# Optimization experiments

Hardware: AMD Instinct MI355X
Metric: run time of the kernel (lower is better)

Reference implementation:

```python
import jax, jax.numpy as jnp
import numpy as np
import math

B, L, NV, PRED = 8, 512, 32, 96
D, PL, STRIDE = 128, 16, 8
E, TOPN, H = 8, 2, 512
P = (L - PL) // STRIDE + 2  # 64 patches (includes replication pad of STRIDE)
BAL_COEF, Z_COEF = 0.01, 0.001


def sinusoid_pe(n, d):
    pos = np.arange(n, dtype=np.float32)[:, None]
    div = np.exp(np.arange(0, d, 2, dtype=np.float32) * -(math.log(10000.0) / d))
    pe = np.zeros((n, d), dtype=np.float32)
    pe[:, 0::2] = np.sin(pos * div)
    pe[:, 1::2] = np.cos(pos * div)
    return jnp.asarray(pe)


def setup_inputs() -> dict:
    key = jax.random.key(0)
    ks = jax.random.split(key, 10)
    return {
        "x_enc": jax.random.normal(ks[0], (B, L, NV), jnp.float32),
        "x_mark_enc": jax.random.normal(ks[1], (B, L, 4), jnp.float32),
        "x_dec": jnp.zeros((B, 144, NV), jnp.float32),
        "x_mark_dec": jnp.zeros((B, 144, 4), jnp.float32),
        "W_patch": jax.random.normal(ks[2], (PL, D), jnp.float32) * 0.05,
        "Wg": jax.random.normal(ks[3], (D, E), jnp.float32) * 0.05,
        "W1": jax.random.normal(ks[4], (E, D, H), jnp.float32) * 0.05,
        "b1": jnp.zeros((E, H), jnp.float32),
        "W2": jax.random.normal(ks[5], (E, H, D), jnp.float32) * 0.05,
        "b2": jnp.zeros((E, D), jnp.float32),
        "W_head": jax.random.normal(ks[6], (D * P, PRED), jnp.float32) * 0.02,
        "b_head": jnp.zeros((PRED,), jnp.float32),
    }


def _forward(x_enc, W_patch, Wg, W1, b1, W2, b2, W_head, b_head):
    # instance norm over time (detached stats, like the torch code)
    means = jax.lax.stop_gradient(jnp.mean(x_enc, axis=1, keepdims=True))
    xc = x_enc - means
    stdev = jax.lax.stop_gradient(
        jnp.sqrt(jnp.mean((x_enc - means) ** 2, axis=1, keepdims=True) + 1e-5))
    xc = xc / stdev
    # [B, NV, L] -> replication pad right by STRIDE -> unfold into patches
    x = jnp.transpose(xc, (0, 2, 1))
    xp = jnp.pad(x, ((0, 0), (0, 0), (0, STRIDE)), mode="edge")
    idx = jnp.arange(P)[:, None] * STRIDE + jnp.arange(PL)[None, :]  # [P, PL]
    patches = xp[:, :, idx]  # [B, NV, P, PL]
    tok = patches.reshape(B * NV, P, PL)
    h = jnp.einsum("tpl,ld->tpd", tok, W_patch) + sinusoid_pe(P, D)[None]
    # ---- MoE over flattened tokens ----
    N = B * NV * P
    xf = h.reshape(N, D)
    logits = xf @ Wg                              # [N, E]
    probs = jax.nn.softmax(logits, axis=-1)
    gates, tops = jax.lax.top_k(probs, TOPN)      # [N, TOPN]
    # dense per-expert FFN (exact GELU, as nn.GELU default)
    eh = jax.nn.gelu(jnp.einsum("nd,edh->neh", xf, W1) + b1, approximate=False)
    eo = jnp.einsum("neh,ehd->ned", eh, W2) + b2  # [N, E, D]
    onehot = jax.nn.one_hot(tops, E, dtype=xf.dtype)          # [N, TOPN, E]
    cw = jnp.einsum("nk,nke->ne", gates, onehot)              # combine weights
    y = jnp.einsum("ne,ned->nd", cw, eo)
    # aux losses: load-balance + router z-loss
    mask = onehot.sum(axis=1)                                  # [N, E]
    balance = E * jnp.sum(jnp.mean(probs, axis=0) * jnp.mean(mask, axis=0)) / TOPN
    zloss = jnp.mean(jax.nn.logsumexp(logits, axis=-1) ** 2)
    aux = BAL_COEF * balance + Z_COEF * zloss
    # ---- head ----
    enc = y.reshape(B, NV, P, D).transpose(0, 1, 3, 2)         # [B, NV, D, P]
    flat = enc.reshape(B, NV, D * P)
    dec = flat @ W_head + b_head                               # [B, NV, PRED]
    dec = jnp.transpose(dec, (0, 2, 1))                        # [B, PRED, NV]
    dec = dec * stdev[:, 0, :][:, None, :] + means[:, 0, :][:, None, :]
    return dec, aux


def reference(x_enc, x_mark_enc, x_dec, x_mark_dec, W_patch, Wg, W1, b1, W2, b2,
              W_head, b_head):
    return _forward(x_enc, W_patch, Wg, W1, b1, W2, b2, W_head, b_head)
```

## Files before the change

kernel.cpp:

```cpp
#include <hip/hip_runtime.h>
#include <math.h>


typedef __attribute__((ext_vector_type(8))) short bf16x8;
typedef __attribute__((ext_vector_type(4))) float f32x4;

__device__ __forceinline__ float bf2f(unsigned short u){
  unsigned x = ((unsigned)u) << 16; float f; __builtin_memcpy(&f, &x, 4); return f;
}
__device__ __forceinline__ unsigned short f2bf(float f){
  unsigned x; __builtin_memcpy(&x, &f, 4);
  return (unsigned short)((x + 0x7FFFu + ((x >> 16) & 1u)) >> 16);
}
__device__ __forceinline__ float ldin(const void* p, int i, int f32){
  return f32 ? ((const float*)p)[i] : bf2f(((const unsigned short*)p)[i]);
}
__device__ __forceinline__ void stout(void* p, int i, float v, int f32){
  if (f32) ((float*)p)[i] = v; else ((unsigned short*)p)[i] = f2bf(v);
}
__device__ __forceinline__ f32x4 mfma16(bf16x8 a, bf16x8 b, f32x4 c){
  return __builtin_amdgcn_mfma_f32_16x16x32_bf16(a, b, c, 0, 0, 0);
}
#define BAR_RAW() asm volatile("s_waitcnt lgkmcnt(0)\n\ts_barrier" ::: "memory")
__device__ __forceinline__ float gelu_fast(float v){
  float u = v*v;
  float inner = v * fmaf(0.044715f, u, 1.0f);
  float e = __expf(-1.5957691216f * inner);
  return v / (1.0f + e);
}

#define OFF_SUMS   64
#define OFF_MEANS  256
#define OFF_STDS   1280
#define OFF_ECNT   2304
#define OFF_W1T    134400
#define OFF_W2T    1182976
#define OFF_WHT    2231552
#define OFF_CW     3804416
#define OFF_XFBF   4328704
#define OFF_FLATB  8523008
#define OFF_EO     12717312
#define OFF_TOKSLOT 79826176
#define OFF_DECP   79957248

__global__ __launch_bounds__(256) void k_prep_tr(const void* __restrict__ W1,
                                                 const void* __restrict__ W2,
                                                 const void* __restrict__ Wh,
                                                 int f32,
                                                 unsigned short* W1T, unsigned short* W2T,
                                                 unsigned short* WhT){
  int t = threadIdx.x;
  __shared__ float tile[32*33];
  int tb = blockIdx.x;
  int r = t >> 3, cg = (t & 7) * 4;
  const void* src; unsigned short* dst;
  int in0, instride, out0, outstride;
  if (tb < 512){
    int e = tb >> 6, ti = tb & 63, d0 = (ti & 3) * 32, h0 = (ti >> 2) * 32;
    src = W1; dst = W1T;
    in0 = e*65536 + d0*512 + h0; instride = 512;
    out0 = e*65536 + h0*128 + d0; outstride = 128;
  } else if (tb < 1024){
    int tc = tb - 512;
    int e = tc >> 6, ti = tc & 63, d0 = (ti & 3) * 32, h0 = (ti >> 2) * 32;
    src = W2; dst = W2T;
    in0 = e*65536 + h0*128 + d0; instride = 128;
    out0 = e*65536 + d0*512 + h0; outstride = 512;
  } else {
    int tc = tb - 1024;
    int kt = tc / 3, nt = tc - kt*3;
    int k0 = kt*32, n0 = nt*32;
    src = Wh; dst = WhT;
    in0 = k0*96 + n0; instride = 96;
    out0 = n0*8192 + k0; outstride = 8192;
  }
  #pragma unroll
  for (int j = 0; j < 4; ++j)
    tile[r*33 + cg + j] = ldin(src, in0 + r*instride + cg + j, f32);
  __syncthreads();
  ushort4 o;
  o.x = f2bf(tile[(cg+0)*33 + r]);
  o.y = f2bf(tile[(cg+1)*33 + r]);
  o.z = f2bf(tile[(cg+2)*33 + r]);
  o.w = f2bf(tile[(cg+3)*33 + r]);
  *(ushort4*)(dst + out0 + r*outstride + cg) = o;
}

__global__ __launch_bounds__(256) void k_embed(const void* __restrict__ xe,
                                               const void* __restrict__ Wp,
                                               const void* __restrict__ Wg,
                                               int f32,
                                               float* means, float* stds,
                                               unsigned short* xfbf, float* cwg,
                                               float* sums,
                                               int* ecnt, int* elist, int* tokslot){
  __shared__ float xn[512];
  __shared__ float WpL[2048];
  __shared__ float WgL[1024];
  __shared__ float Xf[8192];
  __shared__ float lp[1024];
  __shared__ float taux[576];
  __shared__ float reds[256], redss[256];
  __shared__ float msh[2];
  __shared__ int lcnt[8], lbase[8];

  int bv = blockIdx.x;
  int b = bv >> 5, v = bv & 31;
  int t = threadIdx.x;

  if (t < 8) lcnt[t] = 0;

  float x0 = ldin(xe, (b*512 + t)*32 + v, f32);
  float x1 = ldin(xe, (b*512 + t + 256)*32 + v, f32);
  xn[t] = x0; xn[t+256] = x1;
  reds[t] = x0 + x1; redss[t] = x0*x0 + x1*x1;
  #pragma unroll
  for (int it = 0; it < 8; ++it)
    WpL[it*256 + t] = ldin(Wp, it*256 + t, f32);
  #pragma unroll
  for (int j = 0; j < 4; ++j)
    WgL[j*256 + t] = ldin(Wg, j*256 + t, f32);
  __syncthreads();
  for (int s = 128; s > 0; s >>= 1){
    if (t < s){ reds[t] += reds[t+s]; redss[t] += redss[t+s]; }
    __syncthreads();
  }
  if (t == 0){
    float m = reds[0] / 512.f;
    float sd = sqrtf(redss[0] / 512.f - m*m + 1e-5f);
    msh[0] = m; msh[1] = 1.f / sd;
    means[bv] = m; stds[bv] = sd;
  }
  __syncthreads();
  float mean = msh[0], rstd = msh[1];
  xn[t] = (xn[t] - mean) * rstd;
  xn[t+256] = (xn[t+256] - mean) * rstd;
  __syncthreads();
  {
    int p = t >> 2, q = t & 3;
    float tv[16];
    #pragma unroll
    for (int l = 0; l < 16; ++l){
      int xi = p*8 + l; if (xi > 511) xi = 511;
      tv[l] = xn[xi];
    }
    for (int dd = 0; dd < 32; ++dd){
      int d = q*32 + dd;
      float freq = __expf(-(float)(d & ~1) * 0.07195578415606394f);
      float ang = (float)p * freq;
      float acc = (d & 1) ? __cosf(ang) : __sinf(ang);
      #pragma unroll
      for (int l = 0; l < 16; ++l) acc += tv[l] * WpL[l*128 + d];
      Xf[p*128 + d] = acc;
    }
  }
  __syncthreads();
  if (t < 128){
    int p = t >> 1, half = t & 1;
    float s[8] = {0,0,0,0,0,0,0,0};
    for (int d = half*64; d < half*64 + 64; ++d){
      float xv = Xf[p*128 + d];
      #pragma unroll
      for (int e = 0; e < 8; ++e) s[e] += xv * WgL[d*8 + e];
    }
    #pragma unroll
    for (int e = 0; e < 8; ++e) lp[(p*2 + half)*8 + e] = s[e];
  }
  __syncthreads();
  int bi = 0, si = 0, lo0 = 0, lo1 = 0;
  if (t < 64){
    int p = t;
    float lg[8];
    #pragma unroll
    for (int e = 0; e < 8; ++e) lg[e] = lp[(p*2)*8 + e] + lp[(p*2+1)*8 + e];
    float m = lg[0];
    #pragma unroll
    for (int e = 1; e < 8; ++e) m = fmaxf(m, lg[e]);
    float pr[8]; float se = 0.f;
    #pragma unroll
    for (int e = 0; e < 8; ++e){ pr[e] = __expf(lg[e] - m); se += pr[e]; }
    float inv = 1.f / se;
    float lse = m + logf(se);
    #pragma unroll
    for (int e = 0; e < 8; ++e) pr[e] *= inv;
    float best = -1.f;
    #pragma unroll
    for (int e = 0; e < 8; ++e) if (pr[e] > best){ best = pr[e]; bi = e; }
    float sec = -1.f;
    #pragma unroll
    for (int e = 0; e < 8; ++e) if (e != bi && pr[e] > sec){ sec = pr[e]; si = e; }
    #pragma unroll
    for (int e = 0; e < 8; ++e){
      float w = (e == bi) ? best : ((e == si) ? sec : 0.f);
      cwg[(bv*64 + p)*8 + e] = w;
      taux[p*9 + e] = pr[e];
    }
    taux[p*9 + 8] = lse * lse;
    lp[p] = (float)bi; lp[64 + p] = (float)si;
    lo0 = atomicAdd(&lcnt[bi], 1);
    lo1 = atomicAdd(&lcnt[si], 1);
  }
  __syncthreads();
  if (t < 8) lbase[t] = atomicAdd(ecnt + t*32, lcnt[t]);
  __syncthreads();
  if (t < 64){
    int n = bv*64 + t;
    int p0 = lbase[bi] + lo0, p1 = lbase[si] + lo1;
    elist[bi*16384 + p0] = n;
    elist[si*16384 + p1] = n;
    tokslot[n*2]     = (bi << 14) + p0;
    tokslot[n*2 + 1] = (si << 14) + p1;
  }
  if (t < 17){
    float s = 0.f;
    if (t < 8){ for (int p = 0; p < 64; ++p) s += taux[p*9 + t]; }
    else if (t < 16){
      int e = t - 8;
      for (int p = 0; p < 64; ++p)
        s += ((int)lp[p] == e || (int)lp[64+p] == e) ? 1.f : 0.f;
    }
    else { for (int p = 0; p < 64; ++p) s += taux[p*9 + 8]; }
    atomicAdd(sums + t, s);
  }
  #pragma unroll
  for (int pass = 0; pass < 4; ++pass){
    int idx = pass*256 + t;
    int base = idx*8;
    bf16x8 o;
    #pragma unroll
    for (int j = 0; j < 8; ++j) o[j] = (short)f2bf(Xf[base + j]);
    *(bf16x8*)(xfbf + bv*8192 + base) = o;
  }
}

__global__ __launch_bounds__(256, 3) void k_moe(const unsigned short* __restrict__ xfbf,
                                                const unsigned short* __restrict__ W1T,
                                                const unsigned short* __restrict__ W2T,
                                                const void* __restrict__ b1g,
                                                int f32,
                                                const float* __restrict__ cwg,
                                                const int* __restrict__ ecnt,
                                                const int* __restrict__ elist,
                                                float* __restrict__ Eo){
  __shared__ __align__(16) char lds[49664];
  short* Xs  = (short*)(lds);
  short* Bu1 = (short*)(lds + 8704);
  short* Bu2 = (short*)(lds + 26112);
  short* Ag  = (short*)(lds + 44544);
  float* cws = (float*)(lds + 49152);
  int*   lsn = (int*)(lds + 49280);

  int t = threadIdx.x;
  int wave = t >> 6, lane = t & 63;
  int quad = lane >> 4, li = lane & 15;
  int c1 = wave * 16;
  int c2 = wave * 32;

  for (int tb = blockIdx.x; tb < 1536; tb += 768){
    int e = 8, ti = 0;
    {
      int acc = 0;
      #pragma unroll
      for (int ee = 0; ee < 8; ++ee){
        int tl = (ecnt[ee*32] + 31) >> 5;
        if (e == 8 && tb < acc + tl){ e = ee; ti = tb - acc; }
        acc += tl;
      }
    }
    if (e == 8) break;
    int cntE = ecnt[e*32];
    int tbase = ti*32;

    const unsigned short* W1e = W1T + e*65536;
    const unsigned short* W2e = W2T + e*65536;

    bf16x8 pf1[4], pf2[4];
    #pragma unroll
    for (int pass = 0; pass < 4; ++pass){
      int idx = pass*64 + lane;
      int row = idx >> 4, kg = idx & 15;
      pf1[pass] = *(const bf16x8*)(W1e + (c1 + row)*128 + kg*8);
    }
    #pragma unroll
    for (int pass = 0; pass < 4; ++pass){
      int idx = pass*64 + lane;
      int row = idx >> 3, kg = idx & 7;
      pf2[pass] = *(const bf16x8*)(W2e + (c2 + row)*512 + kg*8);
    }

    if (t < 32){
      int ok = (tbase + t) < cntE;
      int n = ok ? elist[e*16384 + tbase + t] : 0;
      lsn[t] = n;
      cws[t] = ok ? cwg[n*8 + e] : 0.f;
    }
    BAR_RAW();
    #pragma unroll
    for (int pass = 0; pass < 2; ++pass){
      int idx = pass*256 + t;
      int row = idx >> 4, kg = idx & 15;
      int n = lsn[row];
      *(bf16x8*)(Xs + row*136 + kg*8) =
        *(const bf16x8*)(xfbf + n*128 + kg*8);
    }
    float cwv[2][4];
    #pragma unroll
    for (int rt = 0; rt < 2; ++rt)
      #pragma unroll
      for (int r = 0; r < 4; ++r)
        cwv[rt][r] = cws[rt*16 + quad*4 + r];
    BAR_RAW();

    f32x4 Yacc[2][2];
    #pragma unroll
    for (int a = 0; a < 2; ++a)
      #pragma unroll
      for (int bb = 0; bb < 2; ++bb){ f32x4 z = {0.f,0.f,0.f,0.f}; Yacc[a][bb] = z; }

    for (int hc = 0; hc < 8; ++hc){
      #pragma unroll
      for (int pass = 0; pass < 4; ++pass){
        int idx = pass*64 + lane;
        int row = idx >> 4, kg = idx & 15;
        *(bf16x8*)(Bu1 + (c1 + row)*136 + kg*8) = pf1[pass];
      }
      #pragma unroll
      for (int pass = 0; pass < 4; ++pass){
        int idx = pass*64 + lane;
        int row = idx >> 3, kg = idx & 7;
        *(bf16x8*)(Bu2 + (c2 + row)*72 + kg*8) = pf2[pass];
      }
      float bias = ldin(b1g, e*512 + hc*64 + c1 + li, f32);
      if (hc < 7){
        #pragma unroll
        for (int pass = 0; pass < 4; ++pass){
          int idx = pass*64 + lane;
          int row = idx >> 4, kg = idx & 15;
          pf1[pass] = *(const bf16x8*)(W1e + ((hc+1)*64 + c1 + row)*128 + kg*8);
        }
        #pragma unroll
        for (int pass = 0; pass < 4; ++pass){
          int idx = pass*64 + lane;
          int row = idx >> 3, kg = idx & 7;
          pf2[pass] = *(const bf16x8*)(W2e + (c2 + row)*512 + (hc+1)*64 + kg*8);
        }
      }
      f32x4 acc1[2];
      { f32x4 z = {0.f,0.f,0.f,0.f}; acc1[0] = z; acc1[1] = z; }
      #pragma unroll
      for (int ks = 0; ks < 4; ++ks){
        int kk = ks*32 + quad*8;
        bf16x8 a0 = *(const bf16x8*)(Xs + li*136 + kk);
        bf16x8 a1 = *(const bf16x8*)(Xs + (16 + li)*136 + kk);
        bf16x8 b0 = *(const bf16x8*)(Bu1 + (c1 + li)*136 + kk);
        acc1[0] = mfma16(a0, b0, acc1[0]);
        acc1[1] = mfma16(a1, b0, acc1[1]);
      }
      BAR_RAW();
      #pragma unroll
      for (int rt = 0; rt < 2; ++rt){
        #pragma unroll
        for (int r = 0; r < 4; ++r){
          int row = rt*16 + quad*4 + r;
          float g = gelu_fast(acc1[rt][r] + bias);
          Ag[row*72 + c1 + li] = (short)f2bf(g * cwv[rt][r]);
        }
      }
      BAR_RAW();
      #pragma unroll
      for (int ks = 0; ks < 2; ++ks){
        int kk = ks*32 + quad*8;
        bf16x8 a0 = *(const bf16x8*)(Ag + li*72 + kk);
        bf16x8 a1 = *(const bf16x8*)(Ag + (16 + li)*72 + kk);
        #pragma unroll
        for (int ct = 0; ct < 2; ++ct){
          bf16x8 bb = *(const bf16x8*)(Bu2 + (c2 + ct*16 + li)*72 + kk);
          Yacc[0][ct] = mfma16(a0, bb, Yacc[0][ct]);
          Yacc[1][ct] = mfma16(a1, bb, Yacc[1][ct]);
        }
      }
    }
    #pragma unroll
    for (int ct = 0; ct < 2; ++ct){
      int col = c2 + ct*16 + li;
      #pragma unroll
      for (int rt = 0; rt < 2; ++rt)
        #pragma unroll
        for (int r = 0; r < 4; ++r){
          int row = rt*16 + quad*4 + r;
          if (tbase + row < cntE)
            Eo[(size_t)((e << 14) + tbase + row)*128 + col] = Yacc[rt][ct][r];
        }
    }
  }
}

__global__ __launch_bounds__(256) void k_flat(const float* __restrict__ Eo,
                                              const int* __restrict__ tokslot,
                                              const float* __restrict__ cwg,
                                              const void* __restrict__ b2g,
                                              int f32,
                                              unsigned short* __restrict__ flatb){
  __shared__ float Yl[64*130];
  __shared__ float b2f[1024];
  __shared__ float cwl[512];
  __shared__ int tsl[128];
  int bv = blockIdx.x;
  int t = threadIdx.x;
  if (t < 64){
    int2 v = *(const int2*)(tokslot + (bv*64 + t)*2);
    tsl[t*2] = v.x; tsl[t*2+1] = v.y;
  }
  #pragma unroll
  for (int j = 0; j < 4; ++j) b2f[j*256 + t] = ldin(b2g, j*256 + t, f32);
  #pragma unroll
  for (int j = 0; j < 2; ++j) cwl[j*256 + t] = cwg[bv*512 + j*256 + t];
  __syncthreads();
  #pragma unroll
  for (int pass = 0; pass < 32; ++pass){
    int idx = pass*256 + t;
    int row = idx >> 7, col = idx & 127;
    Yl[row*130 + col] = Eo[(size_t)tsl[row*2]*128 + col]
                      + Eo[(size_t)tsl[row*2+1]*128 + col];
  }
  __syncthreads();
  int d = t >> 1, ph = (t & 1) * 32;
  float b2c[8];
  #pragma unroll
  for (int e = 0; e < 8; ++e) b2c[e] = b2f[e*128 + d];
  unsigned short ob[32];
  for (int j = 0; j < 32; ++j){
    int p = ph + j;
    float add = 0.f;
    #pragma unroll
    for (int e = 0; e < 8; ++e) add += cwl[p*8 + e] * b2c[e];
    ob[j] = f2bf(Yl[p*130 + d] + add);
  }
  #pragma unroll
  for (int m = 0; m < 4; ++m)
    *(bf16x8*)(flatb + bv*8192 + d*64 + ph + m*8) = *(bf16x8*)(ob + m*8);
}

__global__ __launch_bounds__(256) void k_head(const unsigned short* __restrict__ flatb,
                                              const unsigned short* __restrict__ WhT,
                                              float* __restrict__ dec_part){
  int t = threadIdx.x;
  int mt = blockIdx.x & 15, kc = blockIdx.x >> 4;
  int wave = t >> 6, lane = t & 63, quad = lane >> 4, li = lane & 15;
  int kbase = kc*512 + wave*128;
  f32x4 acc[6];
  #pragma unroll
  for (int nt = 0; nt < 6; ++nt){ f32x4 z = {0.f,0.f,0.f,0.f}; acc[nt] = z; }
  #pragma unroll
  for (int ks = 0; ks < 4; ++ks){
    int k = kbase + ks*32 + quad*8;
    bf16x8 a = *(const bf16x8*)(flatb + (mt*16 + li)*8192 + k);
    #pragma unroll
    for (int nt = 0; nt < 6; ++nt){
      bf16x8 b = *(const bf16x8*)(WhT + (nt*16 + li)*8192 + k);
      acc[nt] = mfma16(a, b, acc[nt]);
    }
  }
  __shared__ float redsh[4][16][96];
  #pragma unroll
  for (int nt = 0; nt < 6; ++nt)
    #pragma unroll
    for (int r = 0; r < 4; ++r)
      redsh[wave][quad*4 + r][nt*16 + li] = acc[nt][r];
  __syncthreads();
  #pragma unroll
  for (int u = 0; u < 6; ++u){
    int o = t*6 + u;
    int row = o / 96, col = o % 96;
    float s = redsh[0][row][col] + redsh[1][row][col] + redsh[2][row][col] + redsh[3][row][col];
    dec_part[kc*24576 + (mt*16 + row)*96 + col] = s;
  }
}

__global__ __launch_bounds__(256) void k_final(const float* __restrict__ dec_part,
                                               const void* __restrict__ bh,
                                               int f32,
                                               const float* __restrict__ means,
                                               const float* __restrict__ stds,
                                               const float* __restrict__ sums,
                                               void* out){
  int o = blockIdx.x*256 + threadIdx.x;
  int b = o / 3072, rem = o % 3072, j = rem >> 5, v = rem & 31;
  int bv = b*32 + v;
  int idx = bv*96 + j;
  float s = 0.f;
  #pragma unroll
  for (int kc = 0; kc < 16; ++kc) s += dec_part[kc*24576 + idx];
  float val = (s + ldin(bh, j, f32)) * stds[bv] + means[bv];
  stout(out, o, val, f32);
  if (o == 0){
    float bal = 0.f;
    for (int e = 0; e < 8; ++e) bal += (sums[e] / 16384.f) * (sums[8+e] / 16384.f);
    bal = 8.f * bal / 2.f;
    float aux = 0.01f * bal + 0.001f * (sums[16] / 16384.f);
    stout(out, 24576, aux, f32);
  }
}

extern "C" void kernel_launch(void* const* d_in, const int* in_sizes, int n_in,
                              void* d_out, int out_size, void* d_ws, size_t ws_size,
                              hipStream_t stream){
  const void* xe = d_in[0];
  const void* Wp = d_in[4];
  const void* Wg = d_in[5];
  const void* W1 = d_in[6];
  const void* b1 = d_in[7];
  const void* W2 = d_in[8];
  const void* b2 = d_in[9];
  const void* Wh = d_in[10];
  const void* bh = d_in[11];

  int f32 = 1;
  if (in_sizes && n_in > 0 && in_sizes[0] == 262144) f32 = 0;

  char* ws = (char*)d_ws;
  float* sums  = (float*)(ws + OFF_SUMS);
  float* means = (float*)(ws + OFF_MEANS);
  float* stds  = (float*)(ws + OFF_STDS);
  int*   ecnt  = (int*)(ws + OFF_ECNT);
  unsigned short* W1T   = (unsigned short*)(ws + OFF_W1T);
  unsigned short* W2T   = (unsigned short*)(ws + OFF_W2T);
  unsigned short* WhT   = (unsigned short*)(ws + OFF_WHT);
  float* cw    = (float*)(ws + OFF_CW);
  unsigned short* xfbf  = (unsigned short*)(ws + OFF_XFBF);
  unsigned short* flatb = (unsigned short*)(ws + OFF_FLATB);
  int*   elist = (int*)(ws + OFF_FLATB);
  float* Eo    = (float*)(ws + OFF_EO);
  int*   tokslot = (int*)(ws + OFF_TOKSLOT);
  float* dec_part = (float*)(ws + OFF_DECP);

  hipMemsetAsync(ws, 0, 3328, stream);
  k_prep_tr<<<1792, 256, 0, stream>>>(W1, W2, Wh, f32, W1T, W2T, WhT);
  k_embed<<<256, 256, 0, stream>>>(xe, Wp, Wg, f32, means, stds,
                                   xfbf, cw, sums, ecnt, elist, tokslot);
  k_moe<<<768, 256, 0, stream>>>(xfbf, W1T, W2T, b1, f32, cw, ecnt, elist, Eo);
  k_flat<<<256, 256, 0, stream>>>(Eo, tokslot, cw, b2, f32, flatb);
  k_head<<<256, 256, 0, stream>>>(flatb, WhT, dec_part);
  k_final<<<96, 256, 0, stream>>>(dec_part, bh, f32, means, stds, sums, d_out);
}
```

Measured before the change: 160.5 us.

## Load W2 fragments directly into registers and launch one MoE tile per block

The MoE kernel stops staging W2 through shared memory and reads the MFMA B-operand fragments for W2 straight from global memory each hidden chunk. This shrinks LDS per block from about 49 KB to about 31 KB, so launch bounds can target 5 blocks per CU. The grid-stride loop over tiles is replaced by one tile per block with a larger grid (1032 blocks, enough for the worst-case tile count). The trade-off is more uncoalesced, latency-exposed global loads of W2 fragments without a prefetch stage, and tighter register limits.

```diff
diff --git a/kernel.cpp b/kernel.cpp
--- a/kernel.cpp
+++ b/kernel.cpp
@@ -233,7 +233,7 @@
   }
 }
 
-__global__ __launch_bounds__(256, 3) void k_moe(const unsigned short* __restrict__ xfbf,
+__global__ __launch_bounds__(256, 5) void k_moe(const unsigned short* __restrict__ xfbf,
                                                 const unsigned short* __restrict__ W1T,
                                                 const unsigned short* __restrict__ W2T,
                                                 const void* __restrict__ b1g,
@@ -242,156 +242,139 @@
                                                 const int* __restrict__ ecnt,
                                                 const int* __restrict__ elist,
                                                 float* __restrict__ Eo){
-  __shared__ __align__(16) char lds[49664];
+  __shared__ __align__(16) char lds[31104];
   short* Xs  = (short*)(lds);
   short* Bu1 = (short*)(lds + 8704);
-  short* Bu2 = (short*)(lds + 26112);
-  short* Ag  = (short*)(lds + 44544);
-  float* cws = (float*)(lds + 49152);
-  int*   lsn = (int*)(lds + 49280);
+  short* Ag  = (short*)(lds + 26112);
+  float* cws = (float*)(lds + 30720);
+  int*   lsn = (int*)(lds + 30848);
 
   int t = threadIdx.x;
+  int e = 8, ti = 0;
+  {
+    int acc = 0, bk = blockIdx.x;
+    #pragma unroll
+    for (int ee = 0; ee < 8; ++ee){
+      int tl = (ecnt[ee*32] + 31) >> 5;
+      if (e == 8 && bk < acc + tl){ e = ee; ti = bk - acc; }
+      acc += tl;
+    }
+  }
+  if (e == 8) return;
+  int cntE = ecnt[e*32];
+  int tbase = ti*32;
+
   int wave = t >> 6, lane = t & 63;
   int quad = lane >> 4, li = lane & 15;
   int c1 = wave * 16;
   int c2 = wave * 32;
 
-  for (int tb = blockIdx.x; tb < 1536; tb += 768){
-    int e = 8, ti = 0;
-    {
-      int acc = 0;
-      #pragma unroll
-      for (int ee = 0; ee < 8; ++ee){
-        int tl = (ecnt[ee*32] + 31) >> 5;
-        if (e == 8 && tb < acc + tl){ e = ee; ti = tb - acc; }
-        acc += tl;
-      }
-    }
-    if (e == 8) break;
-    int cntE = ecnt[e*32];
-    int tbase = ti*32;
-
-    const unsigned short* W1e = W1T + e*65536;
-    const unsigned short* W2e = W2T + e*65536;
-
-    bf16x8 pf1[4], pf2[4];
+  const unsigned short* W1e = W1T + e*65536;
+  const unsigned short* W2e = W2T + e*65536;
+
+  bf16x8 pf1[4];
+  #pragma unroll
+  for (int pass = 0; pass < 4; ++pass){
+    int idx = pass*64 + lane;
+    int row = idx >> 4, kg = idx & 15;
+    pf1[pass] = *(const bf16x8*)(W1e + (c1 + row)*128 + kg*8);
+  }
+
+  if (t < 32){
+    int ok = (tbase + t) < cntE;
+    int n = ok ? elist[e*16384 + tbase + t] : 0;
+    lsn[t] = n;
+    cws[t] = ok ? cwg[n*8 + e] : 0.f;
+  }
+  __syncthreads();
+  #pragma unroll
+  for (int pass = 0; pass < 2; ++pass){
+    int idx = pass*256 + t;
+    int row = idx >> 4, kg = idx & 15;
+    int n = lsn[row];
+    *(bf16x8*)(Xs + row*136 + kg*8) =
+      *(const bf16x8*)(xfbf + n*128 + kg*8);
+  }
+  float cwv[2][4];
+  #pragma unroll
+  for (int rt = 0; rt < 2; ++rt)
+    #pragma unroll
+    for (int r = 0; r < 4; ++r)
+      cwv[rt][r] = cws[rt*16 + quad*4 + r];
+  __syncthreads();
+
+  f32x4 Yacc[2][2];
+  #pragma unroll
+  for (int a = 0; a < 2; ++a)
+    #pragma unroll
+    for (int bb = 0; bb < 2; ++bb){ f32x4 z = {0.f,0.f,0.f,0.f}; Yacc[a][bb] = z; }
+
+  for (int hc = 0; hc < 8; ++hc){
     #pragma unroll
     for (int pass = 0; pass < 4; ++pass){
       int idx = pass*64 + lane;
       int row = idx >> 4, kg = idx & 15;
-      pf1[pass] = *(const bf16x8*)(W1e + (c1 + row)*128 + kg*8);
-    }
-    #pragma unroll
-    for (int pass = 0; pass < 4; ++pass){
-      int idx = pass*64 + lane;
-      int row = idx >> 3, kg = idx & 7;
-      pf2[pass] = *(const bf16x8*)(W2e + (c2 + row)*512 + kg*8);
-    }
-
-    if (t < 32){
-      int ok = (tbase + t) < cntE;
-      int n = ok ? elist[e*16384 + tbase + t] : 0;
-      lsn[t] = n;
-      cws[t] = ok ? cwg[n*8 + e] : 0.f;
-    }
-    BAR_RAW();
-    #pragma unroll
-    for (int pass = 0; pass < 2; ++pass){
-      int idx = pass*256 + t;
-      int row = idx >> 4, kg = idx & 15;
-      int n = lsn[row];
-      *(bf16x8*)(Xs + row*136 + kg*8) =
-        *(const bf16x8*)(xfbf + n*128 + kg*8);
-    }
-    float cwv[2][4];
-    #pragma unroll
-    for (int rt = 0; rt < 2; ++rt)
+      *(bf16x8*)(Bu1 + (c1 + row)*136 + kg*8) = pf1[pass];
+    }
+    float bias = ldin(b1g, e*512 + hc*64 + c1 + li, f32);
+    bf16x8 w2f[2][2];
+    #pragma unroll
+    for (int ks = 0; ks < 2; ++ks)
       #pragma unroll
-      for (int r = 0; r < 4; ++r)
-        cwv[rt][r] = cws[rt*16 + quad*4 + r];
-    BAR_RAW();
-
-    f32x4 Yacc[2][2];
-    #pragma unroll
-    for (int a = 0; a < 2; ++a)
-      #pragma unroll
-      for (int bb = 0; bb < 2; ++bb){ f32x4 z = {0.f,0.f,0.f,0.f}; Yacc[a][bb] = z; }
-
-    for (int hc = 0; hc < 8; ++hc){
+      for (int ct = 0; ct < 2; ++ct)
+        w2f[ks][ct] = *(const bf16x8*)(W2e + (c2 + ct*16 + li)*512 + hc*64 + ks*32 + quad*8);
+    if (hc < 7){
       #pragma unroll
       for (int pass = 0; pass < 4; ++pass){
         int idx = pass*64 + lane;
         int row = idx >> 4, kg = idx & 15;
-        *(bf16x8*)(Bu1 + (c1 + row)*136 + kg*8) = pf1[pass];
+        pf1[pass] = *(const bf16x8*)(W1e + ((hc+1)*64 + c1 + row)*128 + kg*8);
       }
+    }
+    f32x4 acc1[2];
+    { f32x4 z = {0.f,0.f,0.f,0.f}; acc1[0] = z; acc1[1] = z; }
+    #pragma unroll
+    for (int ks = 0; ks < 4; ++ks){
+      int kk = ks*32 + quad*8;
+      bf16x8 a0 = *(const bf16x8*)(Xs + li*136 + kk);
+      bf16x8 a1 = *(const bf16x8*)(Xs + (16 + li)*136 + kk);
+      bf16x8 b0 = *(const bf16x8*)(Bu1 + (c1 + li)*136 + kk);
+      acc1[0] = mfma16(a0, b0, acc1[0]);
+      acc1[1] = mfma16(a1, b0, acc1[1]);
+    }
+    BAR_RAW();
+    #pragma unroll
+    for (int rt = 0; rt < 2; ++rt){
       #pragma unroll
-      for (int pass = 0; pass < 4; ++pass){
-        int idx = pass*64 + lane;
-        int row = idx >> 3, kg = idx & 7;
-        *(bf16x8*)(Bu2 + (c2 + row)*72 + kg*8) = pf2[pass];
+      for (int r = 0; r < 4; ++r){
+        int row = rt*16 + quad*4 + r;
+        float g = gelu_fast(acc1[rt][r] + bias);
+        Ag[row*72 + c1 + li] = (short)f2bf(g * cwv[rt][r]);
       }
-      float bias = ldin(b1g, e*512 + hc*64 + c1 + li, f32);
-      if (hc < 7){
-        #pragma unroll
-        for (int pass = 0; pass < 4; ++pass){
-          int idx = pass*64 + lane;
-          int row = idx >> 4, kg = idx & 15;
-          pf1[pass] = *(const bf16x8*)(W1e + ((hc+1)*64 + c1 + row)*128 + kg*8);
-        }
-        #pragma unroll
-        for (int pass = 0; pass < 4; ++pass){
-          int idx = pass*64 + lane;
-          int row = idx >> 3, kg = idx & 7;
-          pf2[pass] = *(const bf16x8*)(W2e + (c2 + row)*512 + (hc+1)*64 + kg*8);
-        }
+    }
+    BAR_RAW();
+    #pragma unroll
+    for (int ks = 0; ks < 2; ++ks){
+      int kk = ks*32 + quad*8;
+      bf16x8 a0 = *(const bf16x8*)(Ag + li*72 + kk);
+      bf16x8 a1 = *(const bf16x8*)(Ag + (16 + li)*72 + kk);
+      Yacc[0][0] = mfma16(a0, w2f[ks][0], Yacc[0][0]);
+      Yacc[0][1] = mfma16(a0, w2f[ks][1], Yacc[0][1]);
+      Yacc[1][0] = mfma16(a1, w2f[ks][0], Yacc[1][0]);
+      Yacc[1][1] = mfma16(a1, w2f[ks][1], Yacc[1][1]);
+    }
+  }
+  #pragma unroll
+  for (int ct = 0; ct < 2; ++ct){
+    int col = c2 + ct*16 + li;
+    #pragma unroll
+    for (int rt = 0; rt < 2; ++rt)
+      #pragma unroll
+      for (int r = 0; r < 4; ++r){
+        int row = rt*16 + quad*4 + r;
+        if (tbase + row < cntE)
+          Eo[(size_t)((e << 14) + tbase + row)*128 + col] = Yacc[rt][ct][r];
       }
-      f32x4 acc1[2];
-      { f32x4 z = {0.f,0.f,0.f,0.f}; acc1[0] = z; acc1[1] = z; }
-      #pragma unroll
-      for (int ks = 0; ks < 4; ++ks){
-        int kk = ks*32 + quad*8;
-        bf16x8 a0 = *(const bf16x8*)(Xs + li*136 + kk);
-        bf16x8 a1 = *(const bf16x8*)(Xs + (16 + li)*136 + kk);
-        bf16x8 b0 = *(const bf16x8*)(Bu1 + (c1 + li)*136 + kk);
-        acc1[0] = mfma16(a0, b0, acc1[0]);
-        acc1[1] = mfma16(a1, b0, acc1[1]);
-      }
-      BAR_RAW();
-      #pragma unroll
-      for (int rt = 0; rt < 2; ++rt){
-        #pragma unroll
-        for (int r = 0; r < 4; ++r){
-          int row = rt*16 + quad*4 + r;
-          float g = gelu_fast(acc1[rt][r] + bias);
-          Ag[row*72 + c1 + li] = (short)f2bf(g * cwv[rt][r]);
-        }
-      }
-      BAR_RAW();
-      #pragma unroll
-      for (int ks = 0; ks < 2; ++ks){
-        int kk = ks*32 + quad*8;
-        bf16x8 a0 = *(const bf16x8*)(Ag + li*72 + kk);
-        bf16x8 a1 = *(const bf16x8*)(Ag + (16 + li)*72 + kk);
-        #pragma unroll
-        for (int ct = 0; ct < 2; ++ct){
-          bf16x8 bb = *(const bf16x8*)(Bu2 + (c2 + ct*16 + li)*72 + kk);
-          Yacc[0][ct] = mfma16(a0, bb, Yacc[0][ct]);
-          Yacc[1][ct] = mfma16(a1, bb, Yacc[1][ct]);
-        }
-      }
-    }
-    #pragma unroll
-    for (int ct = 0; ct < 2; ++ct){
-      int col = c2 + ct*16 + li;
-      #pragma unroll
-      for (int rt = 0; rt < 2; ++rt)
-        #pragma unroll
-        for (int r = 0; r < 4; ++r){
-          int row = rt*16 + quad*4 + r;
-          if (tbase + row < cntE)
-            Eo[(size_t)((e << 14) + tbase + row)*128 + col] = Yacc[rt][ct][r];
-        }
-    }
   }
 }
 
@@ -538,7 +521,7 @@
   k_prep_tr<<<1792, 256, 0, stream>>>(W1, W2, Wh, f32, W1T, W2T, WhT);
   k_embed<<<256, 256, 0, stream>>>(xe, Wp, Wg, f32, means, stds,
                                    xfbf, cw, sums, ecnt, elist, tokslot);
-  k_moe<<<768, 256, 0, stream>>>(xfbf, W1T, W2T, b1, f32, cw, ecnt, elist, Eo);
+  k_moe<<<1032, 256, 0, stream>>>(xfbf, W1T, W2T, b1, f32, cw, ecnt, elist, Eo);
   k_flat<<<256, 256, 0, stream>>>(Eo, tokslot, cw, b2, f32, flatb);
   k_head<<<256, 256, 0, stream>>>(flatb, WhT, dec_part);
   k_final<<<96, 256, 0, stream>>>(dec_part, bh, f32, means, stds, sums, d_out);
```

Result: slower. 163.8 us (+2.0%).
